# Kernel optimization log

Measured on AMD Instinct MI355X. Metric: run time of the kernel, lower is better.

Reference implementation:

```python
import jax, jax.numpy as jnp
import numpy as np

S, B, I = 512, 64, 1024
H = 1024 // 2  # per-direction hidden (MyBiGRU halves hidden_size)


def _gru(x, h0, Wx, Wh, b):
    """Single-direction GRU, faithful to MyGRU.forward.
    x: (S,B,I); h0: (B,H); Wx: (3,I,H) gates [r,u,h]; Wh: (3,H,H); b: (3,H).
    Note: candidate uses (reset_gate * state) @ Whh, matching torch operator
    precedence in `reset_gate * state @ self.weight_hh`.
    """
    # Precompute all input projections once: (S, 3, B, H)
    xg = jnp.einsum('sbi,gih->sgbh', x, Wx)

    def step(h, xt):
        r = jax.nn.sigmoid(xt[0] + h @ Wh[0] + b[0])
        u = jax.nn.sigmoid(xt[1] + h @ Wh[1] + b[1])
        c = jnp.tanh(xt[2] + (r * h) @ Wh[2] + b[2])
        h_new = u * h + (1.0 - u) * c
        return h_new, h_new

    h_last, hs = jax.lax.scan(step, h0, xg)
    return hs, h_last  # (S,B,H), (B,H)


def setup_inputs() -> dict:
    key = jax.random.key(0)
    ks = jax.random.split(key, 6)
    std = jnp.float32(0.01)
    return {
        "x": jax.random.normal(ks[0], (S, B, I), jnp.float32),
        "initial_state": jax.random.normal(ks[1], (B, 2 * H), jnp.float32),
        "Wx_f": std * jax.random.normal(ks[2], (3, I, H), jnp.float32),
        "Wh_f": std * jax.random.normal(ks[3], (3, H, H), jnp.float32),
        "b_f": jnp.zeros((3, H), jnp.float32),
        "Wx_b": std * jax.random.normal(ks[4], (3, I, H), jnp.float32),
        "Wh_b": std * jax.random.normal(ks[5], (3, H, H), jnp.float32),
        "b_b": jnp.zeros((3, H), jnp.float32),
    }


def reference(x, initial_state, Wx_f, Wh_f, b_f, Wx_b, Wh_b, b_b):
    h0_f = initial_state[:, :H]
    h0_b = initial_state[:, H:]
    fwd_out, fwd_state = _gru(x, h0_f, Wx_f, Wh_f, b_f)
    bwd_out, bwd_state = _gru(x[::-1], h0_b, Wx_b, Wh_b, b_b)
    outputs = jnp.concatenate([fwd_out, bwd_out[::-1]], axis=-1)  # (S,B,2H)
    state = jnp.concatenate([fwd_state, bwd_state], axis=-1)      # (B,2H)
    return outputs, state
```

## Files before the change

kernel.cpp:

```cpp
#include <hip/hip_runtime.h>
#include <hip/hip_bf16.h>


typedef __attribute__((ext_vector_type(8))) short short8;
typedef __attribute__((ext_vector_type(4))) float f32x4;

#define SENT 0x7FC0
#define SENT64 0x7FC07FC07FC07FC0ULL

__device__ __forceinline__ unsigned short f2bf(float f) {
    unsigned u = __builtin_bit_cast(unsigned, f);
    u += 0x7FFFu + ((u >> 16) & 1u);
    return (unsigned short)(u >> 16);
}
__device__ __forceinline__ float bf2f(unsigned short h) {
    unsigned u = ((unsigned)h) << 16;
    return __builtin_bit_cast(float, u);
}


__global__ __launch_bounds__(256) void k_cvt_x(const float* __restrict__ x,
                                               unsigned short* __restrict__ xb) {
    size_t gid = (size_t)blockIdx.x * 256 + threadIdx.x;
    f32x4 a = ((const f32x4*)x)[gid * 2];
    f32x4 b = ((const f32x4*)x)[gid * 2 + 1];
    short8 o;
    o[0] = (short)f2bf(a[0]); o[1] = (short)f2bf(a[1]);
    o[2] = (short)f2bf(a[2]); o[3] = (short)f2bf(a[3]);
    o[4] = (short)f2bf(b[0]); o[5] = (short)f2bf(b[1]);
    o[6] = (short)f2bf(b[2]); o[7] = (short)f2bf(b[3]);
    ((short8*)xb)[gid] = o;
}

__global__ __launch_bounds__(256) void k_cvt_w(const float* __restrict__ Wxf,
                                               const float* __restrict__ Wxb,
                                               unsigned short* __restrict__ wt) {
    int gid = blockIdx.x * 256 + threadIdx.x;
    int n = gid >> 7, kc = gid & 127;
    const float* src = (n < 1536) ? Wxf : Wxb;
    int nn = (n >= 1536) ? n - 1536 : n;
    int g = nn >> 9, h = nn & 511;
    short8 o;
#pragma unroll
    for (int j = 0; j < 8; ++j)
        o[j] = (short)f2bf(src[(size_t)(g * 1024 + kc * 8 + j) * 512 + h]);
    *(short8*)(wt + (size_t)n * 1024 + kc * 8) = o;
}

__global__ __launch_bounds__(256) void k_cvt_whsl(const float* __restrict__ Whf,
                                                  const float* __restrict__ Whb,
                                                  unsigned short* __restrict__ o) {
    int gid = blockIdx.x * 256 + threadIdx.x;
    int kc = gid & 63;
    int r = gid >> 6;
    int c = r & 31; r >>= 5;
    int g = r % 3;  r /= 3;
    int w = r & 15, d = r >> 4;
    const float* src = d ? Whb : Whf;
    short8 v;
#pragma unroll
    for (int j = 0; j < 8; ++j)
        v[j] = (short)f2bf(src[(size_t)(g * 512 + kc * 8 + j) * 512 + w * 32 + c]);
    *(short8*)(o + ((size_t)(((d * 16 + w) * 3 + g) * 32 + c)) * 512 + kc * 8) = v;
}

__global__ __launch_bounds__(256) void k_sent(unsigned short* __restrict__ h4,
                                              unsigned short* __restrict__ rh4) {
    int gid = blockIdx.x * 256 + threadIdx.x;
    short8 s;
#pragma unroll
    for (int j = 0; j < 8; ++j) s[j] = (short)SENT;
    ((short8*)h4)[gid] = s;
    ((short8*)rh4)[gid] = s;
}

__global__ __launch_bounds__(256) void k_init(const float* __restrict__ h0,
                                              unsigned short* __restrict__ h4) {
    int gid = blockIdx.x * 256 + threadIdx.x;
    int b = gid >> 10, ch = gid & 1023;
    int d = ch >> 9, k = ch & 511;
    h4[((size_t)d * 64 + b) * 512 + k] = f2bf(h0[gid]);
}


__global__ __launch_bounds__(256) void k_gemm(const unsigned short* __restrict__ A,
                                              const unsigned short* __restrict__ Bt,
                                              unsigned short* __restrict__ C) {
    __shared__ unsigned short Al[128 * 40];
    __shared__ unsigned short Bl[128 * 40];
    const int n0 = blockIdx.x * 128;
    const int m0 = blockIdx.y * 128;
    const int t = threadIdx.x, wave = t >> 6, lane = t & 63;
    const int lg = lane >> 4, lr = lane & 15;
    const int wm = wave >> 1, wn = wave & 1;
    const int lrow = t >> 2, lkb = t & 3;

    f32x4 acc[4][4] = {};
    for (int kt = 0; kt < 32; ++kt) {
        const int k0 = kt * 32;
#pragma unroll
        for (int p = 0; p < 2; ++p) {
            int row = lrow + p * 64;
            *(short8*)(Al + row * 40 + lkb * 8) =
                *(const short8*)(A + (size_t)(m0 + row) * 1024 + k0 + lkb * 8);
            *(short8*)(Bl + row * 40 + lkb * 8) =
                *(const short8*)(Bt + (size_t)(n0 + row) * 1024 + k0 + lkb * 8);
        }
        __syncthreads();
        short8 af[4], bfr[4];
#pragma unroll
        for (int mi = 0; mi < 4; ++mi)
            af[mi] = *(const short8*)(Al + (wm * 64 + mi * 16 + lr) * 40 + lg * 8);
#pragma unroll
        for (int ni = 0; ni < 4; ++ni)
            bfr[ni] = *(const short8*)(Bl + (wn * 64 + ni * 16 + lr) * 40 + lg * 8);
#pragma unroll
        for (int mi = 0; mi < 4; ++mi)
#pragma unroll
            for (int ni = 0; ni < 4; ++ni)
                acc[mi][ni] = __builtin_amdgcn_mfma_f32_16x16x32_bf16(af[mi], bfr[ni],
                                                                      acc[mi][ni], 0, 0, 0);
        __syncthreads();
    }
#pragma unroll
    for (int mi = 0; mi < 4; ++mi)
#pragma unroll
        for (int ni = 0; ni < 4; ++ni) {
            int m = m0 + wm * 64 + mi * 16 + lg * 4;
            int n = n0 + wn * 64 + ni * 16 + lr;
#pragma unroll
            for (int jj = 0; jj < 4; ++jj)
                C[(size_t)(m + jj) * 3072 + n] = f2bf(acc[mi][ni][jj]);
        }
}


__device__ __forceinline__ void wait_frag(const char* p, short8* fr) {
    for (;;) {
        asm volatile(
            "global_load_dwordx4 %0, %16, off sc1\n\t"
            "global_load_dwordx4 %1, %16, off offset:64 sc1\n\t"
            "global_load_dwordx4 %2, %16, off offset:128 sc1\n\t"
            "global_load_dwordx4 %3, %16, off offset:192 sc1\n\t"
            "global_load_dwordx4 %4, %16, off offset:256 sc1\n\t"
            "global_load_dwordx4 %5, %16, off offset:320 sc1\n\t"
            "global_load_dwordx4 %6, %16, off offset:384 sc1\n\t"
            "global_load_dwordx4 %7, %16, off offset:448 sc1\n\t"
            "global_load_dwordx4 %8, %16, off offset:512 sc1\n\t"
            "global_load_dwordx4 %9, %16, off offset:576 sc1\n\t"
            "global_load_dwordx4 %10, %16, off offset:640 sc1\n\t"
            "global_load_dwordx4 %11, %16, off offset:704 sc1\n\t"
            "global_load_dwordx4 %12, %16, off offset:768 sc1\n\t"
            "global_load_dwordx4 %13, %16, off offset:832 sc1\n\t"
            "global_load_dwordx4 %14, %16, off offset:896 sc1\n\t"
            "global_load_dwordx4 %15, %16, off offset:960 sc1"
            : "=v"(fr[0]), "=v"(fr[1]), "=v"(fr[2]), "=v"(fr[3]),
              "=v"(fr[4]), "=v"(fr[5]), "=v"(fr[6]), "=v"(fr[7]),
              "=v"(fr[8]), "=v"(fr[9]), "=v"(fr[10]), "=v"(fr[11]),
              "=v"(fr[12]), "=v"(fr[13]), "=v"(fr[14]), "=v"(fr[15])
            : "v"(p) : "memory");
        asm volatile("s_waitcnt vmcnt(0)" ::: "memory");
        int bad = 0;
#pragma unroll
        for (int i = 0; i < 16; ++i)
            bad |= (((unsigned short)fr[i][0]) == SENT) |
                   (((unsigned short)fr[i][4]) == SENT);
        if (!__any(bad)) break;
        __builtin_amdgcn_s_sleep(2);
    }
    __builtin_amdgcn_sched_barrier(0);
}


__global__ __launch_bounds__(256) void k_rec(const unsigned short* __restrict__ xg,
                                             const unsigned short* __restrict__ whsl,
                                             const float* __restrict__ h0,
                                             const float* __restrict__ b_f,
                                             const float* __restrict__ b_b,
                                             unsigned long long* h4,
                                             unsigned long long* rh4,
                                             float* __restrict__ out) {
    __shared__ unsigned short Wl[3 * 32 * 512];

    const int blk = blockIdx.x;
    const int d = blk >> 4, w = blk & 15;
    const int t = threadIdx.x;
    const int wave = t >> 6, lane = t & 63;
    const int lg = lane >> 4, lr = lane & 15;

    {
        const char* wsrc = (const char*)(whsl + (size_t)(d * 16 + w) * (3 * 32 * 512));
#pragma unroll
        for (int i = 0; i < 24; ++i) {
            int byte = (t + i * 256) << 4;
            int swz = byte ^ (((byte >> 10) & 7) << 4);
            *(short8*)((char*)Wl + swz) = *(const short8*)(wsrc + byte);
        }
    }
    __syncthreads();

    const float* bias = d ? b_b : b_f;
    const int b = wave * 16 + lr;
    const int cswz = (lr & 7) << 4;

    f32x4 bR[2], bU[2], bC[2];
    float h_own[2][4];
#pragma unroll
    for (int ct = 0; ct < 2; ++ct) {
        int cc = w * 32 + ct * 16 + lg * 4;
        bR[ct] = *(const f32x4*)(bias + cc);
        bU[ct] = *(const f32x4*)(bias + 512 + cc);
        bC[ct] = *(const f32x4*)(bias + 1024 + cc);
        f32x4 v = *(const f32x4*)(h0 + (size_t)b * 1024 + d * 512 + cc);
#pragma unroll
        for (int jj = 0; jj < 4; ++jj) h_own[ct][jj] = v[jj];
    }

    const size_t SLOT = 131072;
    const size_t rowoff = ((size_t)d * 64 + b) * 1024;
    char* hb = (char*)h4;
    char* rb = (char*)rh4;
    const int fro  = lg * 16;
    const int pubo = w * 64 + lg * 8;

    unsigned long long xR[2], xU[2], xC[2];
    {
        const unsigned short* xp = xg + (size_t)(d ? 511 : 0) * (64 * 3072) +
                                   (size_t)b * 3072 + d * 1536 + w * 32 + lg * 4;
#pragma unroll
        for (int ct = 0; ct < 2; ++ct) {
            xR[ct] = *(const unsigned long long*)(xp + ct * 16);
            xU[ct] = *(const unsigned long long*)(xp + 512 + ct * 16);
            xC[ct] = *(const unsigned long long*)(xp + 1024 + ct * 16);
        }
    }

    for (int it = 0; it < 512; ++it) {
        const int s = d ? (511 - it) : it;
        const size_t slot  = (size_t)(it & 3) * SLOT;
        const size_t oslot = (size_t)((it + 3) & 3) * SLOT;

        short8 fr[16];
        wait_frag(hb + slot + rowoff + fro, fr);

        unsigned long long nR[2], nU[2], nC[2];
        if (it + 1 < 512) {
            const unsigned short* xp = xg + (size_t)(d ? 510 - it : it + 1) * (64 * 3072) +
                                       (size_t)b * 3072 + d * 1536 + w * 32 + lg * 4;
#pragma unroll
            for (int ct = 0; ct < 2; ++ct) {
                nR[ct] = *(const unsigned long long*)(xp + ct * 16);
                nU[ct] = *(const unsigned long long*)(xp + 512 + ct * 16);
                nC[ct] = *(const unsigned long long*)(xp + 1024 + ct * 16);
            }
        }

#pragma unroll
        for (int ct = 0; ct < 2; ++ct) {
            __hip_atomic_store((unsigned long long*)(hb + oslot + rowoff + pubo + ct * 32),
                               SENT64, __ATOMIC_RELAXED, __HIP_MEMORY_SCOPE_AGENT);
            __hip_atomic_store((unsigned long long*)(rb + oslot + rowoff + pubo + ct * 32),
                               SENT64, __ATOMIC_RELAXED, __HIP_MEMORY_SCOPE_AGENT);
        }

        f32x4 aR[2] = {{0,0,0,0},{0,0,0,0}}, aU[2] = {{0,0,0,0},{0,0,0,0}};
#pragma unroll
        for (int ks = 0; ks < 16; ++ks) {
            int koff = ks * 64 + lg * 16;
#pragma unroll
            for (int ct = 0; ct < 2; ++ct) {
                short8 w0 = *(const short8*)((const char*)Wl +
                            ((((ct * 16 + lr) << 10) + koff) ^ cswz));
                short8 w1 = *(const short8*)((const char*)Wl +
                            ((((32 + ct * 16 + lr) << 10) + koff) ^ cswz));
                aR[ct] = __builtin_amdgcn_mfma_f32_16x16x32_bf16(w0, fr[ks], aR[ct], 0, 0, 0);
                aU[ct] = __builtin_amdgcn_mfma_f32_16x16x32_bf16(w1, fr[ks], aU[ct], 0, 0, 0);
            }
        }
        float uu[2][4];
#pragma unroll
        for (int ct = 0; ct < 2; ++ct) {
            unsigned long long rhp = 0;
#pragma unroll
            for (int jj = 0; jj < 4; ++jj) {
                float pr = aR[ct][jj] + bf2f((unsigned short)(xR[ct] >> (16 * jj))) + bR[ct][jj];
                float pu = aU[ct][jj] + bf2f((unsigned short)(xU[ct] >> (16 * jj))) + bU[ct][jj];
                float r = 1.f / (1.f + __expf(-pr));
                uu[ct][jj] = 1.f / (1.f + __expf(-pu));
                rhp |= (unsigned long long)f2bf(r * h_own[ct][jj]) << (16 * jj);
            }
            __hip_atomic_store((unsigned long long*)(rb + slot + rowoff + pubo + ct * 32),
                               rhp, __ATOMIC_RELAXED, __HIP_MEMORY_SCOPE_AGENT);
        }

        short8 gr[16];
        wait_frag(rb + slot + rowoff + fro, gr);

        f32x4 aC[2] = {{0,0,0,0},{0,0,0,0}};
#pragma unroll
        for (int ks = 0; ks < 16; ++ks) {
            int koff = ks * 64 + lg * 16;
#pragma unroll
            for (int ct = 0; ct < 2; ++ct) {
                short8 w2 = *(const short8*)((const char*)Wl +
                            ((((64 + ct * 16 + lr) << 10) + koff) ^ cswz));
                aC[ct] = __builtin_amdgcn_mfma_f32_16x16x32_bf16(w2, gr[ks], aC[ct], 0, 0, 0);
            }
        }
        const size_t nslot = (size_t)((it + 1) & 3) * SLOT;
#pragma unroll
        for (int ct = 0; ct < 2; ++ct) {
            f32x4 ov;
            unsigned long long hp = 0;
#pragma unroll
            for (int jj = 0; jj < 4; ++jj) {
                float pc = aC[ct][jj] + bf2f((unsigned short)(xC[ct] >> (16 * jj))) + bC[ct][jj];
                float e = __expf(-2.f * pc);
                float c = 2.f / (1.f + e) - 1.f;
                float hn = uu[ct][jj] * h_own[ct][jj] + (1.f - uu[ct][jj]) * c;
                h_own[ct][jj] = hn;
                ov[jj] = hn;
                hp |= (unsigned long long)f2bf(hn) << (16 * jj);
            }
            __hip_atomic_store((unsigned long long*)(hb + nslot + rowoff + pubo + ct * 32),
                               hp, __ATOMIC_RELAXED, __HIP_MEMORY_SCOPE_AGENT);
            *(f32x4*)(out + ((size_t)s * 64 + b) * 1024 + d * 512 + w * 32 + ct * 16 + lg * 4) = ov;
        }
        if (it + 1 < 512) {
#pragma unroll
            for (int ct = 0; ct < 2; ++ct) { xR[ct] = nR[ct]; xU[ct] = nU[ct]; xC[ct] = nC[ct]; }
        }
    }

#pragma unroll
    for (int ct = 0; ct < 2; ++ct) {
        f32x4 ov = {h_own[ct][0], h_own[ct][1], h_own[ct][2], h_own[ct][3]};
        *(f32x4*)(out + (size_t)33554432 + (size_t)b * 1024 + d * 512 +
                  w * 32 + ct * 16 + lg * 4) = ov;
    }
}


extern "C" void kernel_launch(void* const* d_in, const int* in_sizes, int n_in,
                              void* d_out, int out_size, void* d_ws, size_t ws_size,
                              hipStream_t stream) {
    const float* x   = (const float*)d_in[0];
    const float* h0  = (const float*)d_in[1];
    const float* Wxf = (const float*)d_in[2];
    const float* Whf = (const float*)d_in[3];
    const float* bf_ = (const float*)d_in[4];
    const float* Wxb = (const float*)d_in[5];
    const float* Whb = (const float*)d_in[6];
    const float* bb_ = (const float*)d_in[7];
    float* out = (float*)d_out;

    char* ws = (char*)d_ws;
    size_t off = 0;
    auto take = [&](size_t bytes) {
        char* p = ws + off;
        off += (bytes + 255) & ~(size_t)255;
        return p;
    };
    unsigned short* xb   = (unsigned short*)take((size_t)33554432 * 2);
    unsigned short* wt   = (unsigned short*)take((size_t)3072 * 1024 * 2);
    unsigned short* xgp  = (unsigned short*)take((size_t)32768 * 3072 * 2);
    unsigned short* whsl = (unsigned short*)take((size_t)2 * 16 * 3 * 32 * 512 * 2);
    unsigned long long* h4  = (unsigned long long*)take((size_t)4 * 131072);
    unsigned long long* rh4 = (unsigned long long*)take((size_t)4 * 131072);

    if (off > ws_size) return;

    hipLaunchKernelGGL(k_cvt_x,    dim3(16384),   dim3(256), 0, stream, x, xb);
    hipLaunchKernelGGL(k_cvt_w,    dim3(1536),    dim3(256), 0, stream, Wxf, Wxb, wt);
    hipLaunchKernelGGL(k_cvt_whsl, dim3(768),     dim3(256), 0, stream, Whf, Whb, whsl);
    hipLaunchKernelGGL(k_sent,     dim3(128),     dim3(256), 0, stream,
                       (unsigned short*)h4, (unsigned short*)rh4);
    hipLaunchKernelGGL(k_init,     dim3(256),     dim3(256), 0, stream, h0,
                       (unsigned short*)h4);
    hipLaunchKernelGGL(k_gemm,     dim3(24, 256), dim3(256), 0, stream, xb, wt, xgp);
    hipLaunchKernelGGL(k_rec,      dim3(32),      dim3(256), 0, stream, xgp, whsl, h0,
                       bf_, bb_, h4, rh4, out);
}
```

Measured before the change: 5.696 ms.

## Interleave both GRU directions per block with a producer wave staging input projections

The recurrent kernel changes from one direction per block (16 blocks per direction, 32 hidden columns each) to each of the 32 blocks handling 16 columns for both directions. The forward and backward chains are interleaved within one step so each direction's cross-block wait can overlap the other's compute. A fifth wave is added as a producer that prefetches the next step's input projections into a double-buffered LDS area, with workgroup-scoped ready/ack flags. The GEMM epilogue now writes projections in a step-major layout matched to this access pattern, so each block reads contiguous chunks. The trade-offs are more LDS (both directions' weights), more flag-polling and synchronisation points per step, and a scattered write pattern in the GEMM epilogue.

```diff
diff --git a/kernel.cpp b/kernel.cpp
--- a/kernel.cpp
+++ b/kernel.cpp
@@ -17,6 +17,10 @@
     unsigned u = ((unsigned)h) << 16;
     return __builtin_bit_cast(float, u);
 }
+__device__ __forceinline__ float xv(unsigned long long p, int jj) {
+    return bf2f((unsigned short)(p >> (16 * jj)));
+}
+__device__ __forceinline__ int imin(int a, int b) { return a < b ? a : b; }
 
 
 __global__ __launch_bounds__(256) void k_cvt_x(const float* __restrict__ x,
@@ -53,15 +57,15 @@
     int gid = blockIdx.x * 256 + threadIdx.x;
     int kc = gid & 63;
     int r = gid >> 6;
-    int c = r & 31; r >>= 5;
+    int c = r & 15; r >>= 4;
     int g = r % 3;  r /= 3;
-    int w = r & 15, d = r >> 4;
+    int w = r & 31, d = r >> 5;
     const float* src = d ? Whb : Whf;
     short8 v;
 #pragma unroll
     for (int j = 0; j < 8; ++j)
-        v[j] = (short)f2bf(src[(size_t)(g * 512 + kc * 8 + j) * 512 + w * 32 + c]);
-    *(short8*)(o + ((size_t)(((d * 16 + w) * 3 + g) * 32 + c)) * 512 + kc * 8) = v;
+        v[j] = (short)f2bf(src[(size_t)(g * 512 + kc * 8 + j) * 512 + w * 16 + c]);
+    *(short8*)(o + ((size_t)((d * 32 + w) * 3 + g) * 16 + c) * 512 + kc * 8) = v;
 }
 
 __global__ __launch_bounds__(256) void k_sent(unsigned short* __restrict__ h4,
@@ -128,9 +132,17 @@
         for (int ni = 0; ni < 4; ++ni) {
             int m = m0 + wm * 64 + mi * 16 + lg * 4;
             int n = n0 + wn * 64 + ni * 16 + lr;
-#pragma unroll
-            for (int jj = 0; jj < 4; ++jj)
-                C[(size_t)(m + jj) * 3072 + n] = f2bf(acc[mi][ni][jj]);
+            int dd = n >= 1536;
+            int nn = n - dd * 1536;
+            int g = nn >> 9, h = nn & 511;
+            size_t colbase = (size_t)dd * 98304 + (size_t)(h >> 4) * 3072 +
+                             (size_t)((h >> 2) & 3) * 12 + g * 4 + (h & 3);
+#pragma unroll
+            for (int jj = 0; jj < 4; ++jj) {
+                int mm = m + jj;
+                int s = mm >> 6, brow = mm & 63;
+                C[(size_t)s * 196608 + colbase + (size_t)brow * 48] = f2bf(acc[mi][ni][jj]);
+            }
         }
 }
 
@@ -172,7 +184,7 @@
 }
 
 
-__global__ __launch_bounds__(256) void k_rec(const unsigned short* __restrict__ xg,
+__global__ __launch_bounds__(320) void k_rec(const unsigned short* __restrict__ xgr,
                                              const unsigned short* __restrict__ whsl,
                                              const float* __restrict__ h0,
                                              const float* __restrict__ b_f,
@@ -180,163 +192,236 @@
                                              unsigned long long* h4,
                                              unsigned long long* rh4,
                                              float* __restrict__ out) {
-    __shared__ unsigned short Wl[3 * 32 * 512];
-
-    const int blk = blockIdx.x;
-    const int d = blk >> 4, w = blk & 15;
+    __shared__ char Wlb[98304];
+    __shared__ char xls[24576];
+    __shared__ int xg_ready;
+    __shared__ int xg_ack[4];
+
+    const int w = blockIdx.x;
     const int t = threadIdx.x;
-    const int wave = t >> 6, lane = t & 63;
-    const int lg = lane >> 4, lr = lane & 15;
-
-    {
-        const char* wsrc = (const char*)(whsl + (size_t)(d * 16 + w) * (3 * 32 * 512));
-#pragma unroll
-        for (int i = 0; i < 24; ++i) {
-            int byte = (t + i * 256) << 4;
+    const int wave5 = t >> 6, lane = t & 63;
+
+    if (t == 0) {
+        xg_ready = 0;
+        xg_ack[0] = xg_ack[1] = xg_ack[2] = xg_ack[3] = 0;
+    }
+    for (int i = 0; i < 20; ++i) {
+        int c = t + i * 320;
+        if (c < 6144) {
+            int half = (c >= 3072);
+            int byte = (c - half * 3072) << 4;
             int swz = byte ^ (((byte >> 10) & 7) << 4);
-            *(short8*)((char*)Wl + swz) = *(const short8*)(wsrc + byte);
+            *(short8*)(Wlb + half * 49152 + swz) =
+                *(const short8*)((const char*)whsl + (size_t)(half * 32 + w) * 49152 + byte);
         }
     }
     __syncthreads();
 
-    const float* bias = d ? b_b : b_f;
+    if (wave5 == 4) {
+        for (int it = 0; it < 512; ++it) {
+            if (it >= 2) {
+                for (;;) {
+                    int a0 = __hip_atomic_load(&xg_ack[0], __ATOMIC_RELAXED, __HIP_MEMORY_SCOPE_WORKGROUP);
+                    int a1 = __hip_atomic_load(&xg_ack[1], __ATOMIC_RELAXED, __HIP_MEMORY_SCOPE_WORKGROUP);
+                    int a2 = __hip_atomic_load(&xg_ack[2], __ATOMIC_RELAXED, __HIP_MEMORY_SCOPE_WORKGROUP);
+                    int a3 = __hip_atomic_load(&xg_ack[3], __ATOMIC_RELAXED, __HIP_MEMORY_SCOPE_WORKGROUP);
+                    if (imin(imin(a0, a1), imin(a2, a3)) >= it - 1) break;
+                    __builtin_amdgcn_s_sleep(1);
+                }
+            }
+            const char* pf = (const char*)xgr + (size_t)it * 393216 +
+                             (size_t)w * 6144 + lane * 96;
+            const char* pb = (const char*)xgr + (size_t)(511 - it) * 393216 + 196608 +
+                             (size_t)w * 6144 + lane * 96;
+            short8 vf[6], vb[6];
+#pragma unroll
+            for (int k = 0; k < 6; ++k) {
+                vf[k] = *(const short8*)(pf + k * 16);
+                vb[k] = *(const short8*)(pb + k * 16);
+            }
+            char* dst = xls + (it & 1) * 12288 + lane * 96;
+#pragma unroll
+            for (int k = 0; k < 6; ++k) {
+                *(short8*)(dst + k * 16) = vf[k];
+                *(short8*)(dst + 6144 + k * 16) = vb[k];
+            }
+            __builtin_amdgcn_fence(__ATOMIC_RELEASE, "workgroup");
+            if (lane == 0)
+                __hip_atomic_store(&xg_ready, it + 1, __ATOMIC_RELAXED, __HIP_MEMORY_SCOPE_WORKGROUP);
+        }
+        return;
+    }
+
+    const int wave = wave5, lg = lane >> 4, lr = lane & 15;
     const int b = wave * 16 + lr;
+    const int cc = w * 16 + lg * 4;
     const int cswz = (lr & 7) << 4;
 
-    f32x4 bR[2], bU[2], bC[2];
-    float h_own[2][4];
-#pragma unroll
-    for (int ct = 0; ct < 2; ++ct) {
-        int cc = w * 32 + ct * 16 + lg * 4;
-        bR[ct] = *(const f32x4*)(bias + cc);
-        bU[ct] = *(const f32x4*)(bias + 512 + cc);
-        bC[ct] = *(const f32x4*)(bias + 1024 + cc);
-        f32x4 v = *(const f32x4*)(h0 + (size_t)b * 1024 + d * 512 + cc);
-#pragma unroll
-        for (int jj = 0; jj < 4; ++jj) h_own[ct][jj] = v[jj];
-    }
-
-    const size_t SLOT = 131072;
-    const size_t rowoff = ((size_t)d * 64 + b) * 1024;
-    char* hb = (char*)h4;
-    char* rb = (char*)rh4;
+    const f32x4 bRf = *(const f32x4*)(b_f + cc);
+    const f32x4 bUf = *(const f32x4*)(b_f + 512 + cc);
+    const f32x4 bCf = *(const f32x4*)(b_f + 1024 + cc);
+    const f32x4 bRb = *(const f32x4*)(b_b + cc);
+    const f32x4 bUb = *(const f32x4*)(b_b + 512 + cc);
+    const f32x4 bCb = *(const f32x4*)(b_b + 1024 + cc);
+
+    float hf[4], hbo[4];
+#pragma unroll
+    for (int jj = 0; jj < 4; ++jj) {
+        hf[jj]  = h0[(size_t)b * 1024 + cc + jj];
+        hbo[jj] = h0[(size_t)b * 1024 + 512 + cc + jj];
+    }
+
+    const size_t rof = (size_t)b * 1024;
+    const size_t rob = (size_t)(64 + b) * 1024;
     const int fro  = lg * 16;
-    const int pubo = w * 64 + lg * 8;
-
-    unsigned long long xR[2], xU[2], xC[2];
-    {
-        const unsigned short* xp = xg + (size_t)(d ? 511 : 0) * (64 * 3072) +
-                                   (size_t)b * 3072 + d * 1536 + w * 32 + lg * 4;
-#pragma unroll
-        for (int ct = 0; ct < 2; ++ct) {
-            xR[ct] = *(const unsigned long long*)(xp + ct * 16);
-            xU[ct] = *(const unsigned long long*)(xp + 512 + ct * 16);
-            xC[ct] = *(const unsigned long long*)(xp + 1024 + ct * 16);
-        }
-    }
+    const int pubo = w * 32 + lg * 8;
+    const int xoff = (b * 4 + lg) * 24;
+    char* hbP = (char*)h4;
+    char* rbP = (char*)rh4;
 
     for (int it = 0; it < 512; ++it) {
-        const int s = d ? (511 - it) : it;
-        const size_t slot  = (size_t)(it & 3) * SLOT;
-        const size_t oslot = (size_t)((it + 3) & 3) * SLOT;
+        const size_t slot  = (size_t)(it & 3) << 17;
+        const size_t nslot = (size_t)((it + 1) & 3) << 17;
+        const size_t oslot = (size_t)((it + 3) & 3) << 17;
 
         short8 fr[16];
-        wait_frag(hb + slot + rowoff + fro, fr);
-
-        unsigned long long nR[2], nU[2], nC[2];
-        if (it + 1 < 512) {
-            const unsigned short* xp = xg + (size_t)(d ? 510 - it : it + 1) * (64 * 3072) +
-                                       (size_t)b * 3072 + d * 1536 + w * 32 + lg * 4;
-#pragma unroll
-            for (int ct = 0; ct < 2; ++ct) {
-                nR[ct] = *(const unsigned long long*)(xp + ct * 16);
-                nU[ct] = *(const unsigned long long*)(xp + 512 + ct * 16);
-                nC[ct] = *(const unsigned long long*)(xp + 1024 + ct * 16);
-            }
-        }
-
-#pragma unroll
-        for (int ct = 0; ct < 2; ++ct) {
-            __hip_atomic_store((unsigned long long*)(hb + oslot + rowoff + pubo + ct * 32),
-                               SENT64, __ATOMIC_RELAXED, __HIP_MEMORY_SCOPE_AGENT);
-            __hip_atomic_store((unsigned long long*)(rb + oslot + rowoff + pubo + ct * 32),
-                               SENT64, __ATOMIC_RELAXED, __HIP_MEMORY_SCOPE_AGENT);
-        }
-
-        f32x4 aR[2] = {{0,0,0,0},{0,0,0,0}}, aU[2] = {{0,0,0,0},{0,0,0,0}};
+        wait_frag(hbP + slot + rof + fro, fr);
+        __hip_atomic_store((unsigned long long*)(hbP + oslot + rof + pubo), SENT64,
+                           __ATOMIC_RELAXED, __HIP_MEMORY_SCOPE_AGENT);
+
+        while (__hip_atomic_load(&xg_ready, __ATOMIC_RELAXED, __HIP_MEMORY_SCOPE_WORKGROUP) < it + 1)
+            __builtin_amdgcn_s_sleep(1);
+        __builtin_amdgcn_fence(__ATOMIC_ACQUIRE, "workgroup");
+        const char* xp = xls + (it & 1) * 12288 + xoff;
+        const unsigned long long xfR = *(const unsigned long long*)(xp);
+        const unsigned long long xfU = *(const unsigned long long*)(xp + 8);
+        const unsigned long long xfC = *(const unsigned long long*)(xp + 16);
+        const unsigned long long xbR = *(const unsigned long long*)(xp + 6144);
+        const unsigned long long xbU = *(const unsigned long long*)(xp + 6144 + 8);
+        const unsigned long long xbC = *(const unsigned long long*)(xp + 6144 + 16);
+
+        f32x4 aR = {0.f, 0.f, 0.f, 0.f}, aU = {0.f, 0.f, 0.f, 0.f};
 #pragma unroll
         for (int ks = 0; ks < 16; ++ks) {
             int koff = ks * 64 + lg * 16;
-#pragma unroll
-            for (int ct = 0; ct < 2; ++ct) {
-                short8 w0 = *(const short8*)((const char*)Wl +
-                            ((((ct * 16 + lr) << 10) + koff) ^ cswz));
-                short8 w1 = *(const short8*)((const char*)Wl +
-                            ((((32 + ct * 16 + lr) << 10) + koff) ^ cswz));
-                aR[ct] = __builtin_amdgcn_mfma_f32_16x16x32_bf16(w0, fr[ks], aR[ct], 0, 0, 0);
-                aU[ct] = __builtin_amdgcn_mfma_f32_16x16x32_bf16(w1, fr[ks], aU[ct], 0, 0, 0);
-            }
-        }
-        float uu[2][4];
-#pragma unroll
-        for (int ct = 0; ct < 2; ++ct) {
+            short8 w0 = *(const short8*)(Wlb + (((lr << 10) + koff) ^ cswz));
+            short8 w1 = *(const short8*)(Wlb + ((16384 + (lr << 10) + koff) ^ cswz));
+            aR = __builtin_amdgcn_mfma_f32_16x16x32_bf16(w0, fr[ks], aR, 0, 0, 0);
+            aU = __builtin_amdgcn_mfma_f32_16x16x32_bf16(w1, fr[ks], aU, 0, 0, 0);
+        }
+        float uf[4];
+        {
             unsigned long long rhp = 0;
 #pragma unroll
             for (int jj = 0; jj < 4; ++jj) {
-                float pr = aR[ct][jj] + bf2f((unsigned short)(xR[ct] >> (16 * jj))) + bR[ct][jj];
-                float pu = aU[ct][jj] + bf2f((unsigned short)(xU[ct] >> (16 * jj))) + bU[ct][jj];
+                float pr = aR[jj] + xv(xfR, jj) + bRf[jj];
+                float pu = aU[jj] + xv(xfU, jj) + bUf[jj];
                 float r = 1.f / (1.f + __expf(-pr));
-                uu[ct][jj] = 1.f / (1.f + __expf(-pu));
-                rhp |= (unsigned long long)f2bf(r * h_own[ct][jj]) << (16 * jj);
-            }
-            __hip_atomic_store((unsigned long long*)(rb + slot + rowoff + pubo + ct * 32),
-                               rhp, __ATOMIC_RELAXED, __HIP_MEMORY_SCOPE_AGENT);
-        }
-
-        short8 gr[16];
-        wait_frag(rb + slot + rowoff + fro, gr);
-
-        f32x4 aC[2] = {{0,0,0,0},{0,0,0,0}};
+                uf[jj] = 1.f / (1.f + __expf(-pu));
+                rhp |= (unsigned long long)f2bf(r * hf[jj]) << (16 * jj);
+            }
+            __hip_atomic_store((unsigned long long*)(rbP + slot + rof + pubo), rhp,
+                               __ATOMIC_RELAXED, __HIP_MEMORY_SCOPE_AGENT);
+        }
+
+        short8 fb[16];
+        wait_frag(hbP + slot + rob + fro, fb);
+        __hip_atomic_store((unsigned long long*)(hbP + oslot + rob + pubo), SENT64,
+                           __ATOMIC_RELAXED, __HIP_MEMORY_SCOPE_AGENT);
+
+        f32x4 cR = {0.f, 0.f, 0.f, 0.f}, cU = {0.f, 0.f, 0.f, 0.f};
 #pragma unroll
         for (int ks = 0; ks < 16; ++ks) {
             int koff = ks * 64 + lg * 16;
-#pragma unroll
-            for (int ct = 0; ct < 2; ++ct) {
-                short8 w2 = *(const short8*)((const char*)Wl +
-                            ((((64 + ct * 16 + lr) << 10) + koff) ^ cswz));
-                aC[ct] = __builtin_amdgcn_mfma_f32_16x16x32_bf16(w2, gr[ks], aC[ct], 0, 0, 0);
-            }
-        }
-        const size_t nslot = (size_t)((it + 1) & 3) * SLOT;
-#pragma unroll
-        for (int ct = 0; ct < 2; ++ct) {
+            short8 w0 = *(const short8*)(Wlb + 49152 + (((lr << 10) + koff) ^ cswz));
+            short8 w1 = *(const short8*)(Wlb + 49152 + ((16384 + (lr << 10) + koff) ^ cswz));
+            cR = __builtin_amdgcn_mfma_f32_16x16x32_bf16(w0, fb[ks], cR, 0, 0, 0);
+            cU = __builtin_amdgcn_mfma_f32_16x16x32_bf16(w1, fb[ks], cU, 0, 0, 0);
+        }
+        float ub[4];
+        {
+            unsigned long long rhp = 0;
+#pragma unroll
+            for (int jj = 0; jj < 4; ++jj) {
+                float pr = cR[jj] + xv(xbR, jj) + bRb[jj];
+                float pu = cU[jj] + xv(xbU, jj) + bUb[jj];
+                float r = 1.f / (1.f + __expf(-pr));
+                ub[jj] = 1.f / (1.f + __expf(-pu));
+                rhp |= (unsigned long long)f2bf(r * hbo[jj]) << (16 * jj);
+            }
+            __hip_atomic_store((unsigned long long*)(rbP + slot + rob + pubo), rhp,
+                               __ATOMIC_RELAXED, __HIP_MEMORY_SCOPE_AGENT);
+        }
+
+        short8 gr[16];
+        wait_frag(rbP + slot + rof + fro, gr);
+        __hip_atomic_store((unsigned long long*)(rbP + oslot + rof + pubo), SENT64,
+                           __ATOMIC_RELAXED, __HIP_MEMORY_SCOPE_AGENT);
+
+        f32x4 aC = {0.f, 0.f, 0.f, 0.f};
+#pragma unroll
+        for (int ks = 0; ks < 16; ++ks) {
+            int koff = ks * 64 + lg * 16;
+            short8 w2 = *(const short8*)(Wlb + ((32768 + (lr << 10) + koff) ^ cswz));
+            aC = __builtin_amdgcn_mfma_f32_16x16x32_bf16(w2, gr[ks], aC, 0, 0, 0);
+        }
+        {
             f32x4 ov;
             unsigned long long hp = 0;
 #pragma unroll
             for (int jj = 0; jj < 4; ++jj) {
-                float pc = aC[ct][jj] + bf2f((unsigned short)(xC[ct] >> (16 * jj))) + bC[ct][jj];
+                float pc = aC[jj] + xv(xfC, jj) + bCf[jj];
                 float e = __expf(-2.f * pc);
                 float c = 2.f / (1.f + e) - 1.f;
-                float hn = uu[ct][jj] * h_own[ct][jj] + (1.f - uu[ct][jj]) * c;
-                h_own[ct][jj] = hn;
+                float hn = uf[jj] * hf[jj] + (1.f - uf[jj]) * c;
+                hf[jj] = hn;
                 ov[jj] = hn;
                 hp |= (unsigned long long)f2bf(hn) << (16 * jj);
             }
-            __hip_atomic_store((unsigned long long*)(hb + nslot + rowoff + pubo + ct * 32),
-                               hp, __ATOMIC_RELAXED, __HIP_MEMORY_SCOPE_AGENT);
-            *(f32x4*)(out + ((size_t)s * 64 + b) * 1024 + d * 512 + w * 32 + ct * 16 + lg * 4) = ov;
-        }
-        if (it + 1 < 512) {
-#pragma unroll
-            for (int ct = 0; ct < 2; ++ct) { xR[ct] = nR[ct]; xU[ct] = nU[ct]; xC[ct] = nC[ct]; }
-        }
-    }
-
-#pragma unroll
-    for (int ct = 0; ct < 2; ++ct) {
-        f32x4 ov = {h_own[ct][0], h_own[ct][1], h_own[ct][2], h_own[ct][3]};
-        *(f32x4*)(out + (size_t)33554432 + (size_t)b * 1024 + d * 512 +
-                  w * 32 + ct * 16 + lg * 4) = ov;
+            __hip_atomic_store((unsigned long long*)(hbP + nslot + rof + pubo), hp,
+                               __ATOMIC_RELAXED, __HIP_MEMORY_SCOPE_AGENT);
+            *(f32x4*)(out + ((size_t)it * 64 + b) * 1024 + cc) = ov;
+        }
+
+        short8 gb[16];
+        wait_frag(rbP + slot + rob + fro, gb);
+        __hip_atomic_store((unsigned long long*)(rbP + oslot + rob + pubo), SENT64,
+                           __ATOMIC_RELAXED, __HIP_MEMORY_SCOPE_AGENT);
+
+        f32x4 cC = {0.f, 0.f, 0.f, 0.f};
+#pragma unroll
+        for (int ks = 0; ks < 16; ++ks) {
+            int koff = ks * 64 + lg * 16;
+            short8 w2 = *(const short8*)(Wlb + 49152 + ((32768 + (lr << 10) + koff) ^ cswz));
+            cC = __builtin_amdgcn_mfma_f32_16x16x32_bf16(w2, gb[ks], cC, 0, 0, 0);
+        }
+        {
+            f32x4 ov;
+            unsigned long long hp = 0;
+#pragma unroll
+            for (int jj = 0; jj < 4; ++jj) {
+                float pc = cC[jj] + xv(xbC, jj) + bCb[jj];
+                float e = __expf(-2.f * pc);
+                float c = 2.f / (1.f + e) - 1.f;
+                float hn = ub[jj] * hbo[jj] + (1.f - ub[jj]) * c;
+                hbo[jj] = hn;
+                ov[jj] = hn;
+                hp |= (unsigned long long)f2bf(hn) << (16 * jj);
+            }
+            __hip_atomic_store((unsigned long long*)(hbP + nslot + rob + pubo), hp,
+                               __ATOMIC_RELAXED, __HIP_MEMORY_SCOPE_AGENT);
+            *(f32x4*)(out + ((size_t)(511 - it) * 64 + b) * 1024 + 512 + cc) = ov;
+        }
+
+        if (lane == 0)
+            __hip_atomic_store(&xg_ack[wave], it + 1, __ATOMIC_RELAXED, __HIP_MEMORY_SCOPE_WORKGROUP);
+    }
+
+    {
+        f32x4 of = {hf[0], hf[1], hf[2], hf[3]};
+        f32x4 ob = {hbo[0], hbo[1], hbo[2], hbo[3]};
+        *(f32x4*)(out + (size_t)33554432 + (size_t)b * 1024 + cc) = of;
+        *(f32x4*)(out + (size_t)33554432 + (size_t)b * 1024 + 512 + cc) = ob;
     }
 }
 
@@ -363,8 +448,8 @@
     };
     unsigned short* xb   = (unsigned short*)take((size_t)33554432 * 2);
     unsigned short* wt   = (unsigned short*)take((size_t)3072 * 1024 * 2);
-    unsigned short* xgp  = (unsigned short*)take((size_t)32768 * 3072 * 2);
-    unsigned short* whsl = (unsigned short*)take((size_t)2 * 16 * 3 * 32 * 512 * 2);
+    unsigned short* xgr  = (unsigned short*)take((size_t)512 * 196608 * 2);
+    unsigned short* whsl = (unsigned short*)take((size_t)2 * 32 * 3 * 16 * 512 * 2);
     unsigned long long* h4  = (unsigned long long*)take((size_t)4 * 131072);
     unsigned long long* rh4 = (unsigned long long*)take((size_t)4 * 131072);
 
@@ -377,7 +462,7 @@
                        (unsigned short*)h4, (unsigned short*)rh4);
     hipLaunchKernelGGL(k_init,     dim3(256),     dim3(256), 0, stream, h0,
                        (unsigned short*)h4);
-    hipLaunchKernelGGL(k_gemm,     dim3(24, 256), dim3(256), 0, stream, xb, wt, xgp);
-    hipLaunchKernelGGL(k_rec,      dim3(32),      dim3(256), 0, stream, xgp, whsl, h0,
+    hipLaunchKernelGGL(k_gemm,     dim3(24, 256), dim3(256), 0, stream, xb, wt, xgr);
+    hipLaunchKernelGGL(k_rec,      dim3(32),      dim3(320), 0, stream, xgr, whsl, h0,
                        bf_, bb_, h4, rh4, out);
 }
```

Result: faster. 4.901 ms (median of 2 runs) (-13.9%).
